# Kernel tuning notes

Measured on AMD Instinct MI355X. Metric: run time of the kernel, lower is better.

## Reference

```python
import jax, jax.numpy as jnp
import numpy as np
import math

NUM_HEADS = 16

def get_slopes(n):
    def pow2(n):
        start = 2 ** (-2 ** (-(math.log2(n) - 3)))
        return [start * start ** i for i in range(n)]
    if math.log2(n).is_integer():
        return pow2(n)
    c = 2 ** math.floor(math.log2(n))
    return pow2(c) + get_slopes(2 * c)[0::2][: n - c]


def setup_inputs() -> dict:
    key = jax.random.key(0)
    ks = jax.random.split(key, 5)
    B, T, C = 2, 2048, 1024
    return {
        "x": jax.random.normal(ks[0], (B, T, C), dtype=jnp.float32),
        "W_qkv": jax.random.normal(ks[1], (C, 3 * C), dtype=jnp.float32) * 0.02,
        "b_qkv": jax.random.normal(ks[2], (3 * C,), dtype=jnp.float32) * 0.02,
        "W_proj": jax.random.normal(ks[3], (C, C), dtype=jnp.float32) * 0.02,
        "b_proj": jax.random.normal(ks[4], (C,), dtype=jnp.float32) * 0.02,
    }


def reference(x, W_qkv, b_qkv, W_proj, b_proj):
    B, T, C = x.shape
    H = NUM_HEADS
    D = C // H
    qkv = x @ W_qkv + b_qkv                       # [B,T,3C]
    q, k, v = jnp.split(qkv, 3, axis=-1)
    q = q.reshape(B, T, H, D).transpose(0, 2, 1, 3)  # [B,H,T,D]
    k = k.reshape(B, T, H, D).transpose(0, 2, 1, 3)
    v = v.reshape(B, T, H, D).transpose(0, 2, 1, 3)

    slopes = jnp.asarray(get_slopes(H), dtype=jnp.float32)  # [H]
    idx = jnp.arange(T)
    # alibi_bias(L).T in source: -(i-j) for j<=i, 0 for j>i  == min(j-i, 0)
    alibi = jnp.minimum(idx[None, :] - idx[:, None], 0).astype(jnp.float32)  # [T,T]
    bias = slopes[:, None, None] * alibi          # [H,T,T]

    scale = 1.0 / math.sqrt(D)
    scores = jnp.einsum("bhtd,bhsd->bhts", q, k) * scale + bias[None]
    # NOTE: source code builds a causal -inf mask but never adds it -> non-causal
    w = jax.nn.softmax(scores, axis=-1)
    y = jnp.einsum("bhts,bhsd->bhtd", w, v)       # [B,H,T,D]
    y = y.transpose(0, 2, 1, 3).reshape(B, T, C)
    return y @ W_proj + b_proj
```

## Files before the change

kernel.cpp:

```cpp
#include <hip/hip_runtime.h>
#include <hip/hip_bf16.h>
#include <cmath>
#include <cstdint>

typedef __bf16 bf16_t;
typedef __bf16 bf16x8 __attribute__((ext_vector_type(8)));
typedef float f32x4 __attribute__((ext_vector_type(4)));
typedef float f32x8 __attribute__((ext_vector_type(8)));
typedef float f32x16 __attribute__((ext_vector_type(16)));
typedef unsigned int u32x2 __attribute__((ext_vector_type(2)));
typedef unsigned int u32x4 __attribute__((ext_vector_type(4)));

static_assert(sizeof(bf16x8) == 16, "bf16x8 must be 16B");

#define MFMA16(a, b, c) __builtin_amdgcn_mfma_f32_16x16x32_bf16((a), (b), (c), 0, 0, 0)
#define MFMA32(a, b, c) __builtin_amdgcn_mfma_f32_32x32x16_bf16((a), (b), (c), 0, 0, 0)

__device__ __forceinline__ void load_lds_16B(const bf16_t* gsrc, bf16_t* ldst) {
  __builtin_amdgcn_global_load_lds(
      (const __attribute__((address_space(1))) void*)gsrc,
      (__attribute__((address_space(3))) void*)ldst, 16, 0, 0);
}

__global__ void detect_dtype(const unsigned short* __restrict__ x,
                             int* __restrict__ flag) {
  const int lane = threadIdx.x;
  int cnt = 0;
#pragma unroll
  for (int t = 0; t < 8; ++t) {
    unsigned short u = x[2 * (lane + 64 * t)];
    int e = (u >> 7) & 0xFF;
    cnt += (e >= 90 && e <= 130) ? 1 : 0;
  }
#pragma unroll
  for (int off = 1; off < 64; off <<= 1) cnt += __shfl_xor(cnt, off, 64);
  if (lane == 0) *flag = (cnt < 300) ? 1 : 0;
}

__global__ __launch_bounds__(256) void convert_x(const void* __restrict__ x_,
                                                 bf16_t* __restrict__ xb,
                                                 const int* __restrict__ flagp) {
  const size_t idx = ((size_t)blockIdx.x * 256 + threadIdx.x) * 8;
  if (*flagp) {
    f32x8 v = *(const f32x8*)((const float*)x_ + idx);
    bf16x8 bv;
#pragma unroll
    for (int e = 0; e < 8; ++e) bv[e] = (bf16_t)v[e];
    *(bf16x8*)&xb[idx] = bv;
  } else {
    *(bf16x8*)&xb[idx] = *(const bf16x8*)((const bf16_t*)x_ + idx);
  }
}

__global__ __launch_bounds__(256) void wt_transpose(const void* __restrict__ W_,
                                                    bf16_t* __restrict__ Wt,
                                                    int K, int N,
                                                    const int* __restrict__ flagp) {
  __shared__ bf16_t tile[64 * 72];
  const int is_f32 = *flagp;
  const int tid = threadIdx.x;
  const int k0 = blockIdx.y * 64;
  const int n0 = blockIdx.x * 64;
  const int r = tid >> 3;
  const int c = (tid & 7) * 8;
#pragma unroll
  for (int t = 0; t < 2; ++t) {
    int rr = r + t * 32;
    if (is_f32) {
      const float* W = (const float*)W_;
      f32x8 v = *(const f32x8*)&W[(size_t)(k0 + rr) * N + n0 + c];
      bf16x8 bv;
#pragma unroll
      for (int e = 0; e < 8; ++e) bv[e] = (bf16_t)v[e];
      *(bf16x8*)&tile[rr * 72 + c] = bv;
    } else {
      const bf16_t* W = (const bf16_t*)W_;
      *(bf16x8*)&tile[rr * 72 + c] = *(const bf16x8*)&W[(size_t)(k0 + rr) * N + n0 + c];
    }
  }
  __syncthreads();
#pragma unroll
  for (int t = 0; t < 2; ++t) {
    int rr = r + t * 32;
    bf16x8 v;
#pragma unroll
    for (int e = 0; e < 8; ++e) v[e] = tile[(c + e) * 72 + rr];
    *(bf16x8*)&Wt[(size_t)(n0 + rr) * K + k0 + c] = v;
  }
}

__global__ __launch_bounds__(256, 2) void gemm_bt(
    const bf16_t* __restrict__ A, const bf16_t* __restrict__ Bt,
    const void* __restrict__ bias_, void* __restrict__ C_,
    bf16_t* __restrict__ qb, bf16_t* __restrict__ kb, bf16_t* __restrict__ vt,
    int M, int N, int K, int mode, const int* __restrict__ flagp) {
  __shared__ bf16_t As[128 * 64];
  __shared__ bf16_t Bs[128 * 64];
  const int is_f32 = *flagp;
  const int tid = threadIdx.x;
  const int wave = tid >> 6, lane = tid & 63;
  const int l16 = lane & 15, quad = lane >> 4;
  const int m0 = blockIdx.y * 128, n0 = blockIdx.x * 128;
  const int wm = (wave >> 1) * 64, wn = (wave & 1) * 64;
  const int lr = lane >> 3, lc = (lane & 7) * 8;
  f32x4 acc[4][4] = {};

  for (int k0 = 0; k0 < K; k0 += 64) {
#pragma unroll
    for (int t = 0; t < 4; ++t) {
      const int chunk = wave * 4 + t;
      const int row = chunk * 8 + lr;
      load_lds_16B(&A[(size_t)(m0 + row) * K + k0 + lc], &As[chunk * 512]);
      load_lds_16B(&Bt[(size_t)(n0 + row) * K + k0 + lc], &Bs[chunk * 512]);
    }
    __syncthreads();
#pragma unroll
    for (int ks = 0; ks < 2; ++ks) {
      bf16x8 af[4], bfr[4];
#pragma unroll
      for (int i = 0; i < 4; ++i) {
        af[i]  = *(const bf16x8*)&As[(wm + i * 16 + l16) * 64 + ks * 32 + quad * 8];
        bfr[i] = *(const bf16x8*)&Bs[(wn + i * 16 + l16) * 64 + ks * 32 + quad * 8];
      }
#pragma unroll
      for (int i = 0; i < 4; ++i)
#pragma unroll
        for (int j = 0; j < 4; ++j)
          acc[i][j] = MFMA16(af[i], bfr[j], acc[i][j]);
    }
    __syncthreads();
  }

#pragma unroll
  for (int j = 0; j < 4; ++j) {
    const int n = n0 + wn + j * 16 + l16;
    const float bv = is_f32 ? ((const float*)bias_)[n]
                            : (float)((const bf16_t*)bias_)[n];
    if (mode == 0) {
#pragma unroll
      for (int i = 0; i < 4; ++i)
#pragma unroll
        for (int r = 0; r < 4; ++r) {
          int m = m0 + wm + i * 16 + quad * 4 + r;
          float val = acc[i][j][r] + bv;
          if (is_f32) ((float*)C_)[(size_t)m * N + n] = val;
          else ((bf16_t*)C_)[(size_t)m * N + n] = (bf16_t)val;
        }
    } else {
      const int region = n >> 10;
      const int nn = n & 1023;
      const int hh = nn >> 6, dd = nn & 63;
#pragma unroll
      for (int i = 0; i < 4; ++i)
#pragma unroll
        for (int r = 0; r < 4; ++r) {
          int m = m0 + wm + i * 16 + quad * 4 + r;
          int bb = m >> 11, tt = m & 2047;
          size_t bh = (size_t)(bb * 16 + hh);
          float val = acc[i][j][r] + bv;
          if (region == 0)
            qb[(bh * 2048 + tt) * 64 + dd] = (bf16_t)val;
          else if (region == 1)
            kb[(bh * 2048 + tt) * 64 + dd] = (bf16_t)val;
          else
            vt[bh * 131072 + (size_t)dd * 2048 + tt] = (bf16_t)val;
        }
    }
  }
}

__global__ __launch_bounds__(512, 4) void attn_kernel(
    const bf16_t* __restrict__ qbuf, const bf16_t* __restrict__ kbuf,
    const bf16_t* __restrict__ vT, bf16_t* __restrict__ y) {
  const int T = 2048;
  __shared__ __align__(16) char smem[36864];
  bf16_t* Ks  = (bf16_t*)smem;
  bf16_t* VTs = (bf16_t*)(smem + 18432);

  const int tid = threadIdx.x;
  const int wave = tid >> 6, lane = tid & 63;
  const int g2 = wave >> 2, wp = wave & 3;
  const int l32 = lane & 31, hi = lane >> 5;
  const int bh = blockIdx.y;
  const int b = bh >> 4, h = bh & 15;
  const int i0 = blockIdx.x * 128 + wp * 32;
  const float L2E = 1.44269504088896f;
  const float c1 = 0.125f * L2E;
  const float c2 = exp2f(-0.5f * (float)(h + 1)) * L2E;

  bf16x8 qf[4];
  {
    const bf16_t* qrow = qbuf + ((size_t)bh * T + i0 + l32) * 64 + hi * 8;
#pragma unroll
    for (int kk = 0; kk < 4; ++kk) qf[kk] = *(const bf16x8*)&qrow[kk * 16];
  }

  f32x16 o[2] = {};
  float rsum = 0.f;

  const bf16_t* kbase = kbuf + (size_t)bh * T * 64;
  const bf16_t* vbase = vT + (size_t)bh * 64 * T;
  bf16_t* myKs = Ks + g2 * 4608;
  bf16_t* myVs = VTs + g2 * 4608;

  const int gtid = tid & 255;
  const int sr = gtid >> 3, sc = (gtid & 7) * 8;
  const int jbase = g2 * 1024;
  const float dif = (float)(4 * hi - i0 - l32);

  for (int jj = 0; jj < 1024; jj += 64) {
    const int j0 = jbase + jj;
#pragma unroll
    for (int t = 0; t < 2; ++t) {
      int rr = sr + t * 32;
      *(bf16x8*)&myKs[rr * 72 + sc] = *(const bf16x8*)&kbase[(size_t)(j0 + rr) * 64 + sc];
      *(bf16x8*)&myVs[rr * 72 + sc] = *(const bf16x8*)&vbase[(size_t)rr * T + j0 + sc];
    }
    __syncthreads();

#pragma unroll
    for (int hl = 0; hl < 2; ++hl) {
      const int jblk = j0 + hl * 32;
      f32x16 s = {};
#pragma unroll
      for (int kk = 0; kk < 4; ++kk) {
        bf16x8 kf = *(const bf16x8*)&myKs[(hl * 32 + l32) * 72 + kk * 16 + hi * 8];
        s = MFMA32(kf, qf[kk], s);
      }

      float rs = 0.f;
      if (jblk >= i0 + 31) {
#pragma unroll
        for (int r = 0; r < 16; ++r) {
          float p = exp2f(c1 * s[r]);
          rs += p; s[r] = p;
        }
      } else {
        const float cjb = c2 * ((float)jblk + dif);
        if (jblk + 31 <= i0) {
#pragma unroll
          for (int r = 0; r < 16; ++r) {
            const float kr = (float)((r & 3) + 8 * (r >> 2));
            float p = exp2f(fmaf(c1, s[r], fmaf(c2, kr, cjb)));
            rs += p; s[r] = p;
          }
        } else {
#pragma unroll
          for (int r = 0; r < 16; ++r) {
            const float kr = (float)((r & 3) + 8 * (r >> 2));
            float p = exp2f(fmaf(c1, s[r], fminf(fmaf(c2, kr, cjb), 0.f)));
            rs += p; s[r] = p;
          }
        }
      }
      rsum += rs;

      unsigned int w[8];
#pragma unroll
      for (int q = 0; q < 8; ++q)
        asm("v_cvt_pk_bf16_f32 %0, %1, %2"
            : "=v"(w[q]) : "v"(s[2 * q]), "v"(s[2 * q + 1]));
      u32x2 q02 = __builtin_amdgcn_permlane32_swap(w[0], w[2], false, false);
      u32x2 q13 = __builtin_amdgcn_permlane32_swap(w[1], w[3], false, false);
      u32x2 q46 = __builtin_amdgcn_permlane32_swap(w[4], w[6], false, false);
      u32x2 q57 = __builtin_amdgcn_permlane32_swap(w[5], w[7], false, false);
      u32x4 a0u = {q02[0], q13[0], q02[1], q13[1]};
      u32x4 a1u = {q46[0], q57[0], q46[1], q57[1]};
      bf16x8 af0 = __builtin_bit_cast(bf16x8, a0u);
      bf16x8 af1 = __builtin_bit_cast(bf16x8, a1u);

#pragma unroll
      for (int db = 0; db < 2; ++db) {
        bf16x8 v0 = *(const bf16x8*)&myVs[(db * 32 + l32) * 72 + hl * 32 + hi * 8];
        o[db] = MFMA32(af0, v0, o[db]);
        bf16x8 v1 = *(const bf16x8*)&myVs[(db * 32 + l32) * 72 + hl * 32 + 16 + hi * 8];
        o[db] = MFMA32(af1, v1, o[db]);
      }
    }
    __syncthreads();
  }

  rsum += __shfl_xor(rsum, 32, 64);

  float* exO = (float*)smem;
  float* exR = (float*)(smem + 33280);
  if (g2 == 1) {
    float* myO = exO + wp * (32 * 65);
#pragma unroll
    for (int db = 0; db < 2; ++db)
#pragma unroll
      for (int r = 0; r < 16; ++r) {
        const int row = (r & 3) + 8 * (r >> 2) + 4 * hi;
        myO[row * 65 + db * 32 + l32] = o[db][r];
      }
    if (lane < 32) exR[wp * 32 + lane] = rsum;
  }
  __syncthreads();
  if (g2 == 0) {
    float* myO = exO + wp * (32 * 65);
#pragma unroll
    for (int r = 0; r < 16; ++r) {
      const int row = (r & 3) + 8 * (r >> 2) + 4 * hi;
      const float denom = __shfl(rsum, row, 64) + exR[wp * 32 + row];
      const float rden = 1.0f / denom;
      const int ig = i0 + row;
#pragma unroll
      for (int db = 0; db < 2; ++db) {
        const float val = (o[db][r] + myO[row * 65 + db * 32 + l32]) * rden;
        y[((size_t)(b * 2048 + ig)) * 1024 + h * 64 + db * 32 + l32] = (bf16_t)val;
      }
    }
  }
}

extern "C" void kernel_launch(void* const* d_in, const int* in_sizes, int n_in,
                              void* d_out, int out_size, void* d_ws, size_t ws_size,
                              hipStream_t stream) {
  const void* x     = d_in[0];
  const void* Wqkv  = d_in[1];
  const void* bqkv  = d_in[2];
  const void* Wproj = d_in[3];
  const void* bproj = d_in[4];

  const size_t SEG = (size_t)32 * 2048 * 64;
  bf16_t* ws = (bf16_t*)d_ws;
  bf16_t* qb = ws;
  bf16_t* kb = ws + SEG;
  bf16_t* vt = ws + 2 * SEG;
  bf16_t* yb = ws + 3 * SEG;
  bf16_t* WqkvT  = yb;
  bf16_t* WprojT = qb;
  bf16_t* xb = (bf16_t*)d_out;
  int* flag1 = (int*)((char*)d_ws + (size_t)31 * 1024 * 1024);
  int* flag2 = (int*)((char*)d_ws + (size_t)4 * 1024 * 1024);

  detect_dtype<<<1, 64, 0, stream>>>((const unsigned short*)x, flag1);
  wt_transpose<<<dim3(48, 16), 256, 0, stream>>>(Wqkv, WqkvT, 1024, 3072, flag1);
  convert_x<<<2048, 256, 0, stream>>>(x, xb, flag1);
  gemm_bt<<<dim3(24, 32), 256, 0, stream>>>(xb, WqkvT, bqkv, nullptr, qb, kb, vt,
                                            4096, 3072, 1024, 1, flag1);
  attn_kernel<<<dim3(16, 32), 512, 0, stream>>>(qb, kb, vt, yb);
  detect_dtype<<<1, 64, 0, stream>>>((const unsigned short*)x, flag2);
  wt_transpose<<<dim3(16, 16), 256, 0, stream>>>(Wproj, WprojT, 1024, 1024, flag2);
  gemm_bt<<<dim3(8, 32), 256, 0, stream>>>(yb, WprojT, bproj, d_out,
                                           nullptr, nullptr, nullptr,
                                           4096, 1024, 1024, 0, flag2);
}
```

Before: 221.4 us.

## Double-buffer K/V tiles in LDS with register prefetch and MFMA priority

The attention loop now prefetches the next K and V tile into registers while computing on the current tile, then writes them into a second LDS buffer. This drops one barrier per iteration and hides global load latency behind the MFMA work. It also batches the LDS fragment loads ahead of the MFMA chains and wraps those chains in s_setprio. LDS use doubles to 72KB per block, which may lower occupancy from the launch bound's target of 4 blocks per CU, and register pressure rises from the prefetch registers.

New measurement: 238.7 us. 7.8% more time.

```diff
diff --git a/kernel.cpp b/kernel.cpp
--- a/kernel.cpp
+++ b/kernel.cpp
@@ -173,9 +173,9 @@
     const bf16_t* __restrict__ qbuf, const bf16_t* __restrict__ kbuf,
     const bf16_t* __restrict__ vT, bf16_t* __restrict__ y) {
   const int T = 2048;
-  __shared__ __align__(16) char smem[36864];
-  bf16_t* Ks  = (bf16_t*)smem;
-  bf16_t* VTs = (bf16_t*)(smem + 18432);
+  __shared__ __align__(16) char smem[73728];
+  bf16_t* KsA = (bf16_t*)smem;
+  bf16_t* VsA = (bf16_t*)(smem + 36864);
 
   const int tid = threadIdx.x;
   const int wave = tid >> 6, lane = tid & 63;
@@ -200,33 +200,58 @@
 
   const bf16_t* kbase = kbuf + (size_t)bh * T * 64;
   const bf16_t* vbase = vT + (size_t)bh * 64 * T;
-  bf16_t* myKs = Ks + g2 * 4608;
-  bf16_t* myVs = VTs + g2 * 4608;
+  bf16_t* Kg = KsA + g2 * 2 * 4608;
+  bf16_t* Vg = VsA + g2 * 2 * 4608;
 
   const int gtid = tid & 255;
   const int sr = gtid >> 3, sc = (gtid & 7) * 8;
+  const int wofs = sr * 72 + sc;
   const int jbase = g2 * 1024;
   const float dif = (float)(4 * hi - i0 - l32);
 
-  for (int jj = 0; jj < 1024; jj += 64) {
-    const int j0 = jbase + jj;
-#pragma unroll
-    for (int t = 0; t < 2; ++t) {
-      int rr = sr + t * 32;
-      *(bf16x8*)&myKs[rr * 72 + sc] = *(const bf16x8*)&kbase[(size_t)(j0 + rr) * 64 + sc];
-      *(bf16x8*)&myVs[rr * 72 + sc] = *(const bf16x8*)&vbase[(size_t)rr * T + j0 + sc];
-    }
-    __syncthreads();
+  const bf16_t* kl = kbase + (size_t)sr * 64 + sc;
+  const bf16_t* vl = vbase + (size_t)sr * T + sc;
+
+  {
+    bf16x8 kr0 = *(const bf16x8*)&kl[(size_t)jbase * 64];
+    bf16x8 kr1 = *(const bf16x8*)&kl[(size_t)jbase * 64 + 32 * 64];
+    bf16x8 vr0 = *(const bf16x8*)&vl[jbase];
+    bf16x8 vr1 = *(const bf16x8*)&vl[jbase + 32 * T];
+    *(bf16x8*)&Kg[wofs] = kr0;
+    *(bf16x8*)&Kg[wofs + 32 * 72] = kr1;
+    *(bf16x8*)&Vg[wofs] = vr0;
+    *(bf16x8*)&Vg[wofs + 32 * 72] = vr1;
+  }
+  __syncthreads();
+
+  for (int t = 0; t < 16; ++t) {
+    const int cur = t & 1;
+    const int j0 = jbase + t * 64;
+
+    bf16x8 kr0, kr1, vr0, vr1;
+    if (t < 15) {
+      const int jn = j0 + 64;
+      kr0 = *(const bf16x8*)&kl[(size_t)jn * 64];
+      kr1 = *(const bf16x8*)&kl[(size_t)jn * 64 + 32 * 64];
+      vr0 = *(const bf16x8*)&vl[jn];
+      vr1 = *(const bf16x8*)&vl[jn + 32 * T];
+    }
+
+    const bf16_t* myKs = Kg + cur * 4608;
+    const bf16_t* myVs = Vg + cur * 4608;
 
 #pragma unroll
     for (int hl = 0; hl < 2; ++hl) {
       const int jblk = j0 + hl * 32;
+      bf16x8 kf[4];
+#pragma unroll
+      for (int kk = 0; kk < 4; ++kk)
+        kf[kk] = *(const bf16x8*)&myKs[(hl * 32 + l32) * 72 + kk * 16 + hi * 8];
       f32x16 s = {};
-#pragma unroll
-      for (int kk = 0; kk < 4; ++kk) {
-        bf16x8 kf = *(const bf16x8*)&myKs[(hl * 32 + l32) * 72 + kk * 16 + hi * 8];
-        s = MFMA32(kf, qf[kk], s);
-      }
+      __builtin_amdgcn_s_setprio(1);
+#pragma unroll
+      for (int kk = 0; kk < 4; ++kk) s = MFMA32(kf[kk], qf[kk], s);
+      __builtin_amdgcn_s_setprio(0);
 
       float rs = 0.f;
       if (jblk >= i0 + 31) {
@@ -269,13 +294,28 @@
       bf16x8 af0 = __builtin_bit_cast(bf16x8, a0u);
       bf16x8 af1 = __builtin_bit_cast(bf16x8, a1u);
 
+      bf16x8 vf[4];
 #pragma unroll
       for (int db = 0; db < 2; ++db) {
-        bf16x8 v0 = *(const bf16x8*)&myVs[(db * 32 + l32) * 72 + hl * 32 + hi * 8];
-        o[db] = MFMA32(af0, v0, o[db]);
-        bf16x8 v1 = *(const bf16x8*)&myVs[(db * 32 + l32) * 72 + hl * 32 + 16 + hi * 8];
-        o[db] = MFMA32(af1, v1, o[db]);
-      }
+        vf[db * 2]     = *(const bf16x8*)&myVs[(db * 32 + l32) * 72 + hl * 32 + hi * 8];
+        vf[db * 2 + 1] = *(const bf16x8*)&myVs[(db * 32 + l32) * 72 + hl * 32 + 16 + hi * 8];
+      }
+      __builtin_amdgcn_s_setprio(1);
+#pragma unroll
+      for (int db = 0; db < 2; ++db) {
+        o[db] = MFMA32(af0, vf[db * 2], o[db]);
+        o[db] = MFMA32(af1, vf[db * 2 + 1], o[db]);
+      }
+      __builtin_amdgcn_s_setprio(0);
+    }
+
+    if (t < 15) {
+      bf16_t* wK = Kg + (cur ^ 1) * 4608;
+      bf16_t* wV = Vg + (cur ^ 1) * 4608;
+      *(bf16x8*)&wK[wofs] = kr0;
+      *(bf16x8*)&wK[wofs + 32 * 72] = kr1;
+      *(bf16x8*)&wV[wofs] = vr0;
+      *(bf16x8*)&wV[wofs + 32 * 72] = vr1;
     }
     __syncthreads();
   }
```

## Double-buffer K/V tiles via direct global-to-LDS loads with XOR swizzle

Applied to the files above, without the earlier changes.

Replaces the synchronous register-staged K/V tile copy with async global_load_lds into two LDS buffers, prefetching the next 64-key tile while the current one is computed. The LDS layout switches from padded rows of 72 to unpadded 64-wide rows with an XOR swizzle so fragment reads avoid bank conflicts. It also batches fragment loads before the MFMAs and raises wave priority around them. LDS use grows to 64KB per block, which may cut occupancy below the launch-bounds target.

After: 220.0 us. No clear change (-0.6%).

```diff
diff --git a/kernel.cpp b/kernel.cpp
--- a/kernel.cpp
+++ b/kernel.cpp
@@ -173,14 +173,15 @@
     const bf16_t* __restrict__ qbuf, const bf16_t* __restrict__ kbuf,
     const bf16_t* __restrict__ vT, bf16_t* __restrict__ y) {
   const int T = 2048;
-  __shared__ __align__(16) char smem[36864];
-  bf16_t* Ks  = (bf16_t*)smem;
-  bf16_t* VTs = (bf16_t*)(smem + 18432);
+  __shared__ __align__(16) char smem[65536];
+  bf16_t* KsA = (bf16_t*)smem;
+  bf16_t* VsA = (bf16_t*)(smem + 32768);
 
   const int tid = threadIdx.x;
   const int wave = tid >> 6, lane = tid & 63;
   const int g2 = wave >> 2, wp = wave & 3;
   const int l32 = lane & 31, hi = lane >> 5;
+  const int x7 = l32 & 7;
   const int bh = blockIdx.y;
   const int b = bh >> 4, h = bh & 15;
   const int i0 = blockIdx.x * 128 + wp * 32;
@@ -200,33 +201,60 @@
 
   const bf16_t* kbase = kbuf + (size_t)bh * T * 64;
   const bf16_t* vbase = vT + (size_t)bh * 64 * T;
-  bf16_t* myKs = Ks + g2 * 4608;
-  bf16_t* myVs = VTs + g2 * 4608;
-
-  const int gtid = tid & 255;
-  const int sr = gtid >> 3, sc = (gtid & 7) * 8;
+  bf16_t* Kg = KsA + g2 * 8192;
+  bf16_t* Vg = VsA + g2 * 8192;
+
   const int jbase = g2 * 1024;
   const float dif = (float)(4 * hi - i0 - l32);
 
-  for (int jj = 0; jj < 1024; jj += 64) {
-    const int j0 = jbase + jj;
-#pragma unroll
-    for (int t = 0; t < 2; ++t) {
-      int rr = sr + t * 32;
-      *(bf16x8*)&myKs[rr * 72 + sc] = *(const bf16x8*)&kbase[(size_t)(j0 + rr) * 64 + sc];
-      *(bf16x8*)&myVs[rr * 72 + sc] = *(const bf16x8*)&vbase[(size_t)rr * T + j0 + sc];
-    }
-    __syncthreads();
+  const int lr8 = lane >> 3;
+  const int swz = ((lane & 7) ^ lr8) * 8;
+  const bf16_t* kl0 = kbase + (size_t)(jbase + wp * 16 + lr8) * 64 + swz;
+  const bf16_t* kl1 = kl0 + 8 * 64;
+  const bf16_t* vl0 = vbase + (size_t)(wp * 16 + lr8) * T + jbase + swz;
+  const bf16_t* vl1 = vl0 + (size_t)8 * T;
+  bf16_t* kd0 = Kg + wp * 1024;
+  bf16_t* vd0 = Vg + wp * 1024;
+
+#define STAGE(bufsel, trel)                                         \
+  do {                                                              \
+    const size_t ko_ = (size_t)(trel) * 4096;                       \
+    const size_t vo_ = (size_t)(trel) * 64;                         \
+    bf16_t* kd_ = kd0 + (bufsel) * 4096;                            \
+    bf16_t* vd_ = vd0 + (bufsel) * 4096;                            \
+    load_lds_16B(kl0 + ko_, kd_);                                   \
+    load_lds_16B(kl1 + ko_, kd_ + 512);                             \
+    load_lds_16B(vl0 + vo_, vd_);                                   \
+    load_lds_16B(vl1 + vo_, vd_ + 512);                             \
+  } while (0)
+
+  STAGE(0, 0);
+  __asm__ volatile("s_waitcnt vmcnt(0)" ::: "memory");
+  __syncthreads();
+
+  for (int t = 0; t < 16; ++t) {
+    const int cur = t & 1;
+    const int j0 = jbase + t * 64;
+
+    if (t < 15) STAGE(cur ^ 1, t + 1);
+
+    const bf16_t* myKs = Kg + cur * 4096;
+    const bf16_t* myVs = Vg + cur * 4096;
 
 #pragma unroll
     for (int hl = 0; hl < 2; ++hl) {
       const int jblk = j0 + hl * 32;
+      bf16x8 kf[4];
+#pragma unroll
+      for (int kk = 0; kk < 4; ++kk) {
+        const int R = hl * 32 + l32;
+        kf[kk] = *(const bf16x8*)&myKs[R * 64 + (((kk << 1) + hi) ^ x7) * 8];
+      }
       f32x16 s = {};
-#pragma unroll
-      for (int kk = 0; kk < 4; ++kk) {
-        bf16x8 kf = *(const bf16x8*)&myKs[(hl * 32 + l32) * 72 + kk * 16 + hi * 8];
-        s = MFMA32(kf, qf[kk], s);
-      }
+      __builtin_amdgcn_s_setprio(1);
+#pragma unroll
+      for (int kk = 0; kk < 4; ++kk) s = MFMA32(kf[kk], qf[kk], s);
+      __builtin_amdgcn_s_setprio(0);
 
       float rs = 0.f;
       if (jblk >= i0 + 31) {
@@ -269,16 +297,26 @@
       bf16x8 af0 = __builtin_bit_cast(bf16x8, a0u);
       bf16x8 af1 = __builtin_bit_cast(bf16x8, a1u);
 
+      bf16x8 vf[4];
 #pragma unroll
       for (int db = 0; db < 2; ++db) {
-        bf16x8 v0 = *(const bf16x8*)&myVs[(db * 32 + l32) * 72 + hl * 32 + hi * 8];
-        o[db] = MFMA32(af0, v0, o[db]);
-        bf16x8 v1 = *(const bf16x8*)&myVs[(db * 32 + l32) * 72 + hl * 32 + 16 + hi * 8];
-        o[db] = MFMA32(af1, v1, o[db]);
-      }
-    }
+        const int D = db * 32 + l32;
+        vf[db * 2]     = *(const bf16x8*)&myVs[D * 64 + ((hl * 4 + hi) ^ x7) * 8];
+        vf[db * 2 + 1] = *(const bf16x8*)&myVs[D * 64 + ((hl * 4 + 2 + hi) ^ x7) * 8];
+      }
+      __builtin_amdgcn_s_setprio(1);
+#pragma unroll
+      for (int db = 0; db < 2; ++db) {
+        o[db] = MFMA32(af0, vf[db * 2], o[db]);
+        o[db] = MFMA32(af1, vf[db * 2 + 1], o[db]);
+      }
+      __builtin_amdgcn_s_setprio(0);
+    }
+
+    __asm__ volatile("s_waitcnt vmcnt(0)" ::: "memory");
     __syncthreads();
   }
+#undef STAGE
 
   rsum += __shfl_xor(rsum, 32, 64);
 
```
